# Performance work log

Hardware: AMD Instinct MI355X
Metric: run time of the kernel (lower is better)

Reference implementation:

```python
import jax, jax.numpy as jnp
import numpy as np

N_NODES = 50000
N_EDGES = 800000
IN_DIM = 128
HIDDEN = 64      # out_channels per head (concat=False -> head mean)
HEADS = 2
N_GRAPHS = 64
LN_EPS = 1e-5


def _layer_norm(x, g, b):
    mu = jnp.mean(x, axis=-1, keepdims=True)
    var = jnp.mean((x - mu) ** 2, axis=-1, keepdims=True)
    return (x - mu) * jax.lax.rsqrt(var + LN_EPS) * g + b


def _transformer_conv(x, src, dst, Wq, bq, Wk, bk, Wv, bv, Ws, bs):
    # PyG TransformerConv, concat=False, root_weight=True, beta=False.
    n = x.shape[0]
    q = (x @ Wq + bq).reshape(n, HEADS, -1)[dst]   # [E, H, D] query at target i
    k = (x @ Wk + bk).reshape(n, HEADS, -1)[src]   # [E, H, D] key at source j
    v = (x @ Wv + bv).reshape(n, HEADS, -1)[src]   # [E, H, D] value at source j
    d = q.shape[-1]
    score = jnp.sum(q * k, axis=-1) / jnp.sqrt(jnp.asarray(d, x.dtype))  # [E, H]
    # segment softmax over incoming edges of each target node
    smax = jax.ops.segment_max(score, dst, num_segments=n)
    e = jnp.exp(score - smax[dst])
    denom = jax.ops.segment_sum(e, dst, num_segments=n)
    alpha = e / denom[dst]                                              # [E, H]
    agg = jax.ops.segment_sum(alpha[..., None] * v, dst, num_segments=n)  # [N, H, D]
    out = jnp.mean(agg, axis=1)                     # concat=False -> head mean
    return out + x @ Ws + bs                        # root/skip connection


def setup_inputs() -> dict:
    key = jax.random.key(0)
    ks = jax.random.split(key, 40)
    inp = {}
    inp["x"] = jax.random.normal(ks[0], (N_NODES, IN_DIM), jnp.float32)
    inp["edge_index"] = jax.random.randint(ks[1], (2, N_EDGES), 0, N_NODES, dtype=jnp.int64)
    inp["batch"] = jnp.sort(jax.random.randint(ks[2], (N_NODES,), 0, N_GRAPHS, dtype=jnp.int64))
    dims = [(IN_DIM, HIDDEN), (HIDDEN, HIDDEN), (HIDDEN, HIDDEN)]
    i = 3
    for l, (din, dout) in enumerate(dims):
        for nm in ("q", "k", "v"):
            inp[f"W{nm}{l}"] = jax.random.normal(ks[i], (din, HEADS * dout), jnp.float32) * 0.05; i += 1
            inp[f"b{nm}{l}"] = jnp.zeros((HEADS * dout,), jnp.float32)
        inp[f"Ws{l}"] = jax.random.normal(ks[i], (din, dout), jnp.float32) * 0.05; i += 1
        inp[f"bs{l}"] = jnp.zeros((dout,), jnp.float32)
    for l in range(2):  # LayerNorm after layers 0 and 1 only
        inp[f"g{l}"] = jnp.ones((HIDDEN,), jnp.float32)
        inp[f"beta{l}"] = jnp.zeros((HIDDEN,), jnp.float32)
    inp["Wp"] = jax.random.normal(ks[i], (HIDDEN, 1), jnp.float32) * 0.05
    inp["bp"] = jnp.zeros((1,), jnp.float32)
    return inp


def reference(x, edge_index, batch,
              Wq0, bq0, Wk0, bk0, Wv0, bv0, Ws0, bs0,
              Wq1, bq1, Wk1, bk1, Wv1, bv1, Ws1, bs1,
              Wq2, bq2, Wk2, bk2, Wv2, bv2, Ws2, bs2,
              g0, beta0, g1, beta1, Wp, bp):
    src, dst = edge_index[0], edge_index[1]
    layers = [(Wq0, bq0, Wk0, bk0, Wv0, bv0, Ws0, bs0),
              (Wq1, bq1, Wk1, bk1, Wv1, bv1, Ws1, bs1),
              (Wq2, bq2, Wk2, bk2, Wv2, bv2, Ws2, bs2)]
    lns = [(g0, beta0), (g1, beta1)]
    h = x
    for i, p in enumerate(layers):
        h = _transformer_conv(h, src, dst, *p)
        h = jax.nn.relu(h)  # dropout p=0.0 / eval -> identity
        if i != len(layers) - 1:
            h = _layer_norm(h, *lns[i])
    # global mean pool per graph
    cnt = jax.ops.segment_sum(jnp.ones((h.shape[0],), h.dtype), batch, num_segments=N_GRAPHS)
    pooled = jax.ops.segment_sum(h, batch, num_segments=N_GRAPHS) / jnp.maximum(cnt, 1.0)[:, None]
    return pooled @ Wp + bp
```

## Files before the change

kernel.cpp:

```cpp
#include <hip/hip_runtime.h>
#include <hip/hip_fp16.h>
#include <math.h>

#define HIDDEN 64
#define HEADS 2
#define NCOLS 448
#define KV_COLS 256
#define N_GRAPHS 64
#define LN_EPS 1e-5f
#define Q_SCALE 0.18033688011112042f

typedef _Float16 half8 __attribute__((ext_vector_type(8)));
typedef _Float16 half2v __attribute__((ext_vector_type(2)));
typedef float    f32x4 __attribute__((ext_vector_type(4)));


__global__ void cast_f2h_kernel(const float* __restrict__ in, _Float16* __restrict__ out, int n4)
{
    int i = blockIdx.x * 256 + threadIdx.x;
    if (i < n4) {
        float4 v = *(const float4*)&in[i * 4];
        __half2 a = __floats2half2_rn(v.x, v.y);
        __half2 b = __floats2half2_rn(v.z, v.w);
        uint2 pk;
        pk.x = *(unsigned int*)&a;
        pk.y = *(unsigned int*)&b;
        *(uint2*)&out[i * 4] = pk;
    }
}

__global__ void pack_kernel(const float* __restrict__ Wq, const float* __restrict__ Wk,
                            const float* __restrict__ Wv, const float* __restrict__ Ws,
                            const float* __restrict__ bq, const float* __restrict__ bk,
                            const float* __restrict__ bv, const float* __restrict__ bs,
                            _Float16* __restrict__ Bt, float* __restrict__ bcat, int K)
{
    int idx = blockIdx.x * 256 + threadIdx.x;
    int total = NCOLS * K;
    if (idx < total) {
        int c = idx / K, k = idx - c * K;
        float v;
        if      (c < 128) v = Wq[k * 128 + c] * Q_SCALE;
        else if (c < 256) v = Wk[k * 128 + (c - 128)];
        else if (c < 384) v = Wv[k * 128 + (c - 256)];
        else              v = Ws[k * 64  + (c - 384)];
        Bt[idx] = (_Float16)v;
    }
    if (idx < NCOLS) {
        float b;
        if      (idx < 128) b = bq[idx] * Q_SCALE;
        else if (idx < 256) b = bk[idx - 128];
        else if (idx < 384) b = bv[idx - 256];
        else                b = bs[idx - 384];
        bcat[idx] = b;
    }
}

template<int K, int NT>
__device__ __forceinline__ void gemm_body(
    const _Float16* __restrict__ Ah, const float* __restrict__ bias,
    _Float16* __restrict__ qh, float* __restrict__ qsk, __half* __restrict__ kvh,
    const _Float16* Bs, int M, int colBase, int chunkRow0, int tid)
{
    int lane = tid & 63;
    int w    = tid >> 6;
    int fr   = lane & 15;
    int g    = lane >> 4;
    int row0 = chunkRow0 + w * 16;
    int arow = row0 + fr;
    if (arow > M - 1) arow = M - 1;

    f32x4 acc[NT];
    #pragma unroll
    for (int c = 0; c < NT; ++c) acc[c] = (f32x4){0.f, 0.f, 0.f, 0.f};

    #pragma unroll
    for (int ks = 0; ks < K / 32; ++ks) {
        int k0 = ks * 32 + g * 8;
        half8 af = *(const half8*)&Ah[(size_t)arow * K + k0];
        #pragma unroll
        for (int c = 0; c < NT; ++c) {
            int rl   = c * 16 + fr;
            int byte = rl * (K * 2) + k0 * 2;
            int sw   = byte ^ ((rl & 7) << 4);
            half8 bf = *(const half8*)((const char*)Bs + sw);
            acc[c] = __builtin_amdgcn_mfma_f32_16x16x32_f16(af, bf, acc[c], 0, 0, 0);
        }
    }

    #pragma unroll
    for (int c = 0; c < NT; ++c) {
        int col = colBase + c * 16 + fr;
        float bs = bias[col];
        #pragma unroll
        for (int j = 0; j < 4; ++j) {
            int row = row0 + g * 4 + j;
            if (row >= M) continue;
            float o = acc[c][j] + bs;
            if (col < 128) {
                qh[(size_t)row * 128 + col] = (_Float16)o;
            } else if (col >= 384) {
                qsk[(size_t)row * 64 + (col - 384)] = o;
            } else {
                int cc  = col - 128;
                int mat = cc >> 7;
                int hh  = (cc >> 6) & 1;
                int d   = cc & 63;
                int pos = mat * 128 + (d >> 2) * 8 + hh * 4 + (d & 3);
                kvh[(size_t)row * KV_COLS + pos] = __float2half_rn(o);
            }
        }
    }
}

template<int K>
__global__ __launch_bounds__(512, 4) void gemm_mfma_kernel(
    const _Float16* __restrict__ Ah,
    const _Float16* __restrict__ Bt,
    const float* __restrict__ bias,
    _Float16* __restrict__ qh, float* __restrict__ qsk,
    __half* __restrict__ kvh, int M)
{
    __shared__ _Float16 Bs[256 * K];

    int tid    = threadIdx.x;
    int colblk = blockIdx.x & 1;
    int chunk  = blockIdx.x >> 1;
    int colBase = colblk ? 256 : 0;
    int cols    = colblk ? 192 : 256;

    int bytes = cols * K * 2;
    const char* src = (const char*)Bt + (size_t)colBase * K * 2;
    for (int i = tid * 16; i < bytes; i += 512 * 16) {
        int rl = i / (K * 2);
        int sw = i ^ ((rl & 7) << 4);
        *(half8*)((char*)Bs + sw) = *(const half8*)(src + i);
    }
    __syncthreads();

    if (colblk == 0)
        gemm_body<K, 16>(Ah, bias, qh, qsk, kvh, Bs, M, 0,   chunk * 128, tid);
    else
        gemm_body<K, 12>(Ah, bias, qh, qsk, kvh, Bs, M, 256, chunk * 128, tid);
}

__global__ void hist_kernel(const int* __restrict__ dst, int* __restrict__ counts, int E)
{
    int i = blockIdx.x * 256 + threadIdx.x;
    if (i < E) atomicAdd(&counts[dst[i]], 1);
}

__global__ __launch_bounds__(256) void block_reduce_kernel(
    const int* __restrict__ counts, int* __restrict__ bsum, int N)
{
    __shared__ int s[256];
    int t = threadIdx.x;
    int i = blockIdx.x * 256 + t;
    s[t] = (i < N) ? counts[i] : 0;
    __syncthreads();
    #pragma unroll
    for (int o = 128; o; o >>= 1) {
        if (t < o) s[t] += s[t + o];
        __syncthreads();
    }
    if (t == 0) bsum[blockIdx.x] = s[0];
}

__global__ __launch_bounds__(256) void scan_partials_kernel(
    const int* __restrict__ bsum, int* __restrict__ boff, int nb, int* __restrict__ rowN)
{
    __shared__ int s[256];
    int t = threadIdx.x;
    int v = (t < nb) ? bsum[t] : 0;
    s[t] = v;
    __syncthreads();
    #pragma unroll
    for (int o = 1; o < 256; o <<= 1) {
        int x = (t >= o) ? s[t - o] : 0;
        __syncthreads();
        s[t] += x;
        __syncthreads();
    }
    if (t < nb) boff[t] = s[t] - v;
    if (t == nb - 1) rowN[0] = s[t];
}

__global__ __launch_bounds__(256) void block_scan_kernel(
    const int* __restrict__ counts, const int* __restrict__ boff,
    int* __restrict__ row_ptr, int* __restrict__ cursor, int N)
{
    __shared__ int s[256];
    int t = threadIdx.x;
    int i = blockIdx.x * 256 + t;
    int v = (i < N) ? counts[i] : 0;
    s[t] = v;
    __syncthreads();
    #pragma unroll
    for (int o = 1; o < 256; o <<= 1) {
        int x = (t >= o) ? s[t - o] : 0;
        __syncthreads();
        s[t] += x;
        __syncthreads();
    }
    if (i < N) {
        int excl = s[t] - v + boff[blockIdx.x];
        row_ptr[i] = excl;
        cursor[i]  = excl;
    }
}

__global__ void scatter_kernel(const int* __restrict__ ei, int* __restrict__ cursor,
                               int* __restrict__ src_sorted, int E)
{
    int i = blockIdx.x * 256 + threadIdx.x;
    if (i < E) {
        int d = ei[E + i];
        int pos = atomicAdd(&cursor[d], 1);
        src_sorted[pos] = ei[i];
    }
}

__device__ __forceinline__ float dpp_sum16(float x)
{
    float t;
    t = __int_as_float(__builtin_amdgcn_mov_dpp(__float_as_int(x), 0xB1,  0xF, 0xF, true)); x += t;
    t = __int_as_float(__builtin_amdgcn_mov_dpp(__float_as_int(x), 0x4E,  0xF, 0xF, true)); x += t;
    t = __int_as_float(__builtin_amdgcn_mov_dpp(__float_as_int(x), 0x141, 0xF, 0xF, true)); x += t;
    t = __int_as_float(__builtin_amdgcn_mov_dpp(__float_as_int(x), 0x140, 0xF, 0xF, true)); x += t;
    return x;
}

__global__ __launch_bounds__(256) void edge_conv_kernel(
    const _Float16* __restrict__ qh, const float* __restrict__ qsk,
    const __half* __restrict__ kvh,
    const int* __restrict__ row_ptr, const int* __restrict__ src_sorted,
    const float* __restrict__ gamma, const float* __restrict__ beta,
    float* __restrict__ hout, _Float16* __restrict__ hh, int N, int do_ln)
{
    int wave = threadIdx.x >> 6;
    int lane = threadIdx.x & 63;
    int g    = lane >> 4;
    int sub  = lane & 15;
    int node = blockIdx.x * 4 + wave;
    if (node >= N) return;

    const _Float16* qrow = qh + (size_t)node * 128;
    uint2 q0p = *(const uint2*)&qrow[sub * 4];
    uint2 q1p = *(const uint2*)&qrow[64 + sub * 4];
    const half2v* q0v = (const half2v*)&q0p;
    const half2v* q1v = (const half2v*)&q1p;

    int e0 = row_ptr[node], e1 = row_ptr[node + 1];
    int deg = e1 - e0;

    float  m0 = -1e30f, m1 = -1e30f;
    float  s0 = 0.f, s1 = 0.f;
    float4 a0 = make_float4(0.f, 0.f, 0.f, 0.f);
    float4 a1 = make_float4(0.f, 0.f, 0.f, 0.f);

    int  e    = e0 + g;
    bool have = (e < e1);
    uint4 kraw, vraw;
    if (have) {
        int j = src_sorted[e];
        const __half* jb = kvh + (size_t)j * KV_COLS;
        kraw = *(const uint4*)&jb[sub * 8];
        vraw = *(const uint4*)&jb[128 + sub * 8];
    }

    while (have) {
        int  en    = e + 4;
        bool haven = (en < e1);
        uint4 krn, vrn;
        if (haven) {
            int jn = src_sorted[en];
            const __half* jbn = kvh + (size_t)jn * KV_COLS;
            krn = *(const uint4*)&jbn[sub * 8];
            vrn = *(const uint4*)&jbn[128 + sub * 8];
        }

        const half2v* kh = (const half2v*)&kraw;
        float p0 = __builtin_amdgcn_fdot2(q0v[0], kh[0],
                     __builtin_amdgcn_fdot2(q0v[1], kh[1], 0.f, false), false);
        float p1 = __builtin_amdgcn_fdot2(q1v[0], kh[2],
                     __builtin_amdgcn_fdot2(q1v[1], kh[3], 0.f, false), false);
        float sc0 = dpp_sum16(p0);
        float sc1 = dpp_sum16(p1);

        const __half2* vp = (const __half2*)&vraw;
        float2 va = __half22float2(vp[0]), vb = __half22float2(vp[1]);
        float2 vc = __half22float2(vp[2]), vd = __half22float2(vp[3]);

        float nm0 = fmaxf(m0, sc0);
        float f0  = exp2f(m0 - nm0);
        float w0  = exp2f(sc0 - nm0);
        s0 = fmaf(s0, f0, w0);
        a0.x = fmaf(a0.x, f0, w0 * va.x);
        a0.y = fmaf(a0.y, f0, w0 * va.y);
        a0.z = fmaf(a0.z, f0, w0 * vb.x);
        a0.w = fmaf(a0.w, f0, w0 * vb.y);
        m0 = nm0;

        float nm1 = fmaxf(m1, sc1);
        float f1  = exp2f(m1 - nm1);
        float w1  = exp2f(sc1 - nm1);
        s1 = fmaf(s1, f1, w1);
        a1.x = fmaf(a1.x, f1, w1 * vc.x);
        a1.y = fmaf(a1.y, f1, w1 * vc.y);
        a1.z = fmaf(a1.z, f1, w1 * vd.x);
        a1.w = fmaf(a1.w, f1, w1 * vd.y);
        m1 = nm1;

        kraw = krn; vraw = vrn; e = en; have = haven;
    }

    #pragma unroll
    for (int offm = 16; offm <= 32; offm <<= 1) {
        float mo0 = __shfl_xor(m0, offm);
        float so0 = __shfl_xor(s0, offm);
        float4 ao0;
        ao0.x = __shfl_xor(a0.x, offm); ao0.y = __shfl_xor(a0.y, offm);
        ao0.z = __shfl_xor(a0.z, offm); ao0.w = __shfl_xor(a0.w, offm);
        float nm = fmaxf(m0, mo0);
        float fa = exp2f(m0 - nm), fb = exp2f(mo0 - nm);
        s0 = s0 * fa + so0 * fb;
        a0.x = a0.x * fa + ao0.x * fb; a0.y = a0.y * fa + ao0.y * fb;
        a0.z = a0.z * fa + ao0.z * fb; a0.w = a0.w * fa + ao0.w * fb;
        m0 = nm;

        float mo1 = __shfl_xor(m1, offm);
        float so1 = __shfl_xor(s1, offm);
        float4 ao1;
        ao1.x = __shfl_xor(a1.x, offm); ao1.y = __shfl_xor(a1.y, offm);
        ao1.z = __shfl_xor(a1.z, offm); ao1.w = __shfl_xor(a1.w, offm);
        nm = fmaxf(m1, mo1);
        fa = exp2f(m1 - nm); fb = exp2f(mo1 - nm);
        s1 = s1 * fa + so1 * fb;
        a1.x = a1.x * fa + ao1.x * fb; a1.y = a1.y * fa + ao1.y * fb;
        a1.z = a1.z * fa + ao1.z * fb; a1.w = a1.w * fa + ao1.w * fb;
        m1 = nm;
    }

    float4 skip = *(const float4*)&qsk[(size_t)node * 64 + sub * 4];
    float4 o;
    if (deg > 0) {
        float r0 = 0.5f / s0, r1 = 0.5f / s1;
        o.x = a0.x * r0 + a1.x * r1 + skip.x;
        o.y = a0.y * r0 + a1.y * r1 + skip.y;
        o.z = a0.z * r0 + a1.z * r1 + skip.z;
        o.w = a0.w * r0 + a1.w * r1 + skip.w;
    } else {
        o = skip;
    }
    o.x = fmaxf(o.x, 0.f); o.y = fmaxf(o.y, 0.f);
    o.z = fmaxf(o.z, 0.f); o.w = fmaxf(o.w, 0.f);

    if (do_ln) {
        float mu = dpp_sum16(o.x + o.y + o.z + o.w) * (1.0f / 64.0f);
        float dx = o.x - mu, dy = o.y - mu, dz = o.z - mu, dw = o.w - mu;
        float var = dpp_sum16(dx * dx + dy * dy + dz * dz + dw * dw) * (1.0f / 64.0f);
        float rs = rsqrtf(var + LN_EPS);
        float4 gm = *(const float4*)&gamma[sub * 4];
        float4 bt = *(const float4*)&beta[sub * 4];
        o.x = dx * rs * gm.x + bt.x;
        o.y = dy * rs * gm.y + bt.y;
        o.z = dz * rs * gm.z + bt.z;
        o.w = dw * rs * gm.w + bt.w;
    }
    if (g == 0) {
        *(float4*)&hout[(size_t)node * HIDDEN + sub * 4] = o;
        __half2 h01 = __floats2half2_rn(o.x, o.y);
        __half2 h23 = __floats2half2_rn(o.z, o.w);
        uint2 pk;
        pk.x = *(unsigned int*)&h01;
        pk.y = *(unsigned int*)&h23;
        *(uint2*)&hh[(size_t)node * HIDDEN + sub * 4] = pk;
    }
}

#define POOL_CHUNK 32
__global__ __launch_bounds__(64) void pool_kernel(const float* __restrict__ h,
                                                  const int* __restrict__ batch,
                                                  float* __restrict__ pooled,
                                                  float* __restrict__ cnt, int N)
{
    int lane = threadIdx.x;
    int start = blockIdx.x * POOL_CHUNK;
    if (start >= N) return;
    int end = min(start + POOL_CHUNK, N);
    int b0 = batch[start];
    int b1 = batch[end - 1];

    if (b0 == b1) {
        float acc = 0.f;
        #pragma unroll 4
        for (int i = start; i < end; ++i)
            acc += h[(size_t)i * HIDDEN + lane];
        atomicAdd(&pooled[b0 * HIDDEN + lane], acc);
        if (lane == 0) atomicAdd(&cnt[b0], (float)(end - start));
    } else {
        float acc = 0.f;
        int cur = b0, c = 0;
        for (int i = start; i < end; ++i) {
            int b = batch[i];
            if (b != cur) {
                atomicAdd(&pooled[cur * HIDDEN + lane], acc);
                if (lane == 0) atomicAdd(&cnt[cur], (float)c);
                acc = 0.f; c = 0; cur = b;
            }
            acc += h[(size_t)i * HIDDEN + lane];
            ++c;
        }
        atomicAdd(&pooled[cur * HIDDEN + lane], acc);
        if (lane == 0) atomicAdd(&cnt[cur], (float)c);
    }
}

__global__ void final_kernel(const float* __restrict__ pooled, const float* __restrict__ cnt,
                             const float* __restrict__ Wp, const float* __restrict__ bp,
                             float* __restrict__ out)
{
    int g = threadIdx.x;
    float c = fmaxf(cnt[g], 1.0f);
    float s = 0.f;
    for (int d = 0; d < HIDDEN; ++d) s += pooled[g * HIDDEN + d] * Wp[d];
    out[g] = s / c + bp[0];
}

extern "C" void kernel_launch(void* const* d_in, const int* in_sizes, int n_in,
                              void* d_out, int out_size, void* d_ws, size_t ws_size,
                              hipStream_t stream)
{
    const float* x    = (const float*)d_in[0];
    const int*   ei   = (const int*)d_in[1];
    const int*   batch= (const int*)d_in[2];

    const float* Wl[3][4];
    const float* bl[3][4];
    for (int l = 0; l < 3; ++l) {
        int b = 3 + l * 8;
        Wl[l][0] = (const float*)d_in[b + 0]; bl[l][0] = (const float*)d_in[b + 1];
        Wl[l][1] = (const float*)d_in[b + 2]; bl[l][1] = (const float*)d_in[b + 3];
        Wl[l][2] = (const float*)d_in[b + 4]; bl[l][2] = (const float*)d_in[b + 5];
        Wl[l][3] = (const float*)d_in[b + 6]; bl[l][3] = (const float*)d_in[b + 7];
    }
    const float* g0    = (const float*)d_in[27];
    const float* beta0 = (const float*)d_in[28];
    const float* g1    = (const float*)d_in[29];
    const float* beta1 = (const float*)d_in[30];
    const float* Wp    = (const float*)d_in[31];
    const float* bp    = (const float*)d_in[32];

    const int N = in_sizes[0] / 128;
    const int E = in_sizes[1] / 2;

    size_t off = 0;
    auto carve = [&](size_t bytes) -> char* {
        char* p = (char*)d_ws + off;
        off = (off + bytes + 255) & ~(size_t)255;
        return p;
    };
    _Float16*  qh     = (_Float16*)carve((size_t)N * 128 * 2);
    float*     qsk    = (float*)carve((size_t)N * 64 * 4);
    __half*    kvh    = (__half*)carve((size_t)N * KV_COLS * 2);
    float*     h      = (float*)carve((size_t)N * HIDDEN * 4);
    _Float16*  hh     = (_Float16*)carve((size_t)N * HIDDEN * 2);
    _Float16*  xh     = (_Float16*)carve((size_t)N * 128 * 2);
    _Float16*  Bt     = (_Float16*)carve((size_t)NCOLS * 128 * 2);
    float*     bcat   = (float*)carve(NCOLS * 4);
    int*       counts = (int*)carve((size_t)N * 4);
    int*       row_ptr= (int*)carve((size_t)(N + 1) * 4);
    int*       cursor = (int*)carve((size_t)N * 4);
    int*       src_sorted = (int*)carve((size_t)E * 4);
    int*       bsum   = (int*)carve(1024 * 4);
    int*       boff   = (int*)carve(1024 * 4);
    float*     pooled = (float*)carve((size_t)(N_GRAPHS * HIDDEN + N_GRAPHS) * 4);
    float*     cntf   = pooled + N_GRAPHS * HIDDEN;

    const int nb = (N + 255) / 256;

    hipMemsetAsync(counts, 0, (size_t)N * 4, stream);
    hist_kernel<<<(E + 255) / 256, 256, 0, stream>>>(ei + E, counts, E);
    block_reduce_kernel<<<nb, 256, 0, stream>>>(counts, bsum, N);
    scan_partials_kernel<<<1, 256, 0, stream>>>(bsum, boff, nb, &row_ptr[N]);
    block_scan_kernel<<<nb, 256, 0, stream>>>(counts, boff, row_ptr, cursor, N);
    scatter_kernel<<<(E + 255) / 256, 256, 0, stream>>>(ei, cursor, src_sorted, E);

    {
        int n4 = (N * 128) / 4;
        cast_f2h_kernel<<<(n4 + 255) / 256, 256, 0, stream>>>(x, xh, n4);
    }

    const int gemm_grid = 2 * ((N + 127) / 128);

    for (int l = 0; l < 3; ++l) {
        int K = (l == 0) ? 128 : 64;
        int packTot = NCOLS * K;
        pack_kernel<<<(packTot + 255) / 256, 256, 0, stream>>>(
            Wl[l][0], Wl[l][1], Wl[l][2], Wl[l][3],
            bl[l][0], bl[l][1], bl[l][2], bl[l][3], Bt, bcat, K);
        if (l == 0)
            gemm_mfma_kernel<128><<<gemm_grid, 512, 0, stream>>>(xh, Bt, bcat, qh, qsk, kvh, N);
        else
            gemm_mfma_kernel<64><<<gemm_grid, 512, 0, stream>>>(hh, Bt, bcat, qh, qsk, kvh, N);
        int do_ln = (l < 2) ? 1 : 0;
        const float* gg = (l == 0) ? g0 : g1;
        const float* bb = (l == 0) ? beta0 : beta1;
        edge_conv_kernel<<<(N + 3) / 4, 256, 0, stream>>>(
            qh, qsk, kvh, row_ptr, src_sorted, gg, bb, h, hh, N, do_ln);
    }

    hipMemsetAsync(pooled, 0, (size_t)(N_GRAPHS * HIDDEN + N_GRAPHS) * 4, stream);
    pool_kernel<<<(N + POOL_CHUNK - 1) / POOL_CHUNK, 64, 0, stream>>>(h, batch, pooled, cntf, N);
    final_kernel<<<1, 64, 0, stream>>>(pooled, cntf, Wp, bp, (float*)d_out);
}
```

Before: 421.3 us.

## Process nodes in descending-degree order and precompute byte offsets for KV gathers

Adds a degree counting-sort that builds a node order from high to low in-degree, and the edge kernel then processes nodes in that order so waves within a block do similar amounts of work and long nodes start first. Source indices are stored as precomputed byte offsets to save address arithmetic in the gather loop. The q·k dot product moves from packed fp16 fdot2 to fp32 FMAs after converting halves. This adds three small kernels plus a serial 64-entry offset pass, and gives up memory locality for q rows and the per-node outputs.

```diff
diff --git a/kernel.cpp b/kernel.cpp
--- a/kernel.cpp
+++ b/kernel.cpp
@@ -6,12 +6,12 @@
 #define HEADS 2
 #define NCOLS 448
 #define KV_COLS 256
+#define KV_ROW_BYTES 512
 #define N_GRAPHS 64
 #define LN_EPS 1e-5f
 #define Q_SCALE 0.18033688011112042f
 
 typedef _Float16 half8 __attribute__((ext_vector_type(8)));
-typedef _Float16 half2v __attribute__((ext_vector_type(2)));
 typedef float    f32x4 __attribute__((ext_vector_type(4)));
 
 
@@ -210,13 +210,52 @@
 }
 
 __global__ void scatter_kernel(const int* __restrict__ ei, int* __restrict__ cursor,
-                               int* __restrict__ src_sorted, int E)
+                               int* __restrict__ src_off, int E)
 {
     int i = blockIdx.x * 256 + threadIdx.x;
     if (i < E) {
         int d = ei[E + i];
         int pos = atomicAdd(&cursor[d], 1);
-        src_sorted[pos] = ei[i];
+        src_off[pos] = ei[i] * KV_ROW_BYTES;
+    }
+}
+
+__global__ __launch_bounds__(256) void deg_hist_kernel(
+    const int* __restrict__ row_ptr, int* __restrict__ dhist, int N)
+{
+    __shared__ int lh[64];
+    int t = threadIdx.x;
+    if (t < 64) lh[t] = 0;
+    __syncthreads();
+    int i = blockIdx.x * 256 + t;
+    if (i < N) {
+        int d = min(row_ptr[i + 1] - row_ptr[i], 63);
+        atomicAdd(&lh[d], 1);
+    }
+    __syncthreads();
+    if (t < 64 && lh[t] > 0) atomicAdd(&dhist[t], lh[t]);
+}
+
+__global__ void deg_offsets_kernel(const int* __restrict__ dhist, int* __restrict__ dcursor)
+{
+    if (threadIdx.x == 0) {
+        int off = 0;
+        for (int d = 63; d >= 0; --d) {
+            dcursor[d] = off;
+            off += dhist[d];
+        }
+    }
+}
+
+__global__ void deg_scatter_kernel(const int* __restrict__ row_ptr,
+                                   int* __restrict__ dcursor,
+                                   int* __restrict__ order, int N)
+{
+    int i = blockIdx.x * 256 + threadIdx.x;
+    if (i < N) {
+        int d = min(row_ptr[i + 1] - row_ptr[i], 63);
+        int pos = atomicAdd(&dcursor[d], 1);
+        order[pos] = i;
     }
 }
 
@@ -232,8 +271,8 @@
 
 __global__ __launch_bounds__(256) void edge_conv_kernel(
     const _Float16* __restrict__ qh, const float* __restrict__ qsk,
-    const __half* __restrict__ kvh,
-    const int* __restrict__ row_ptr, const int* __restrict__ src_sorted,
+    const __half* __restrict__ kvh, const int* __restrict__ order,
+    const int* __restrict__ row_ptr, const int* __restrict__ src_off,
     const float* __restrict__ gamma, const float* __restrict__ beta,
     float* __restrict__ hout, _Float16* __restrict__ hh, int N, int do_ln)
 {
@@ -241,14 +280,22 @@
     int lane = threadIdx.x & 63;
     int g    = lane >> 4;
     int sub  = lane & 15;
-    int node = blockIdx.x * 4 + wave;
-    if (node >= N) return;
-
-    const _Float16* qrow = qh + (size_t)node * 128;
-    uint2 q0p = *(const uint2*)&qrow[sub * 4];
-    uint2 q1p = *(const uint2*)&qrow[64 + sub * 4];
-    const half2v* q0v = (const half2v*)&q0p;
-    const half2v* q1v = (const half2v*)&q1p;
+    int idx  = blockIdx.x * 4 + wave;
+    if (idx >= N) return;
+    int node = order[idx];
+
+    const __half* qrow = (const __half*)(qh + (size_t)node * 128);
+    float4 q0, q1;
+    {
+        uint2 p0 = *(const uint2*)&qrow[sub * 4];
+        uint2 p1 = *(const uint2*)&qrow[64 + sub * 4];
+        const __half2* h0 = (const __half2*)&p0;
+        const __half2* h1 = (const __half2*)&p1;
+        float2 a = __half22float2(h0[0]), b = __half22float2(h0[1]);
+        float2 c = __half22float2(h1[0]), d = __half22float2(h1[1]);
+        q0 = make_float4(a.x, a.y, b.x, b.y);
+        q1 = make_float4(c.x, c.y, d.x, d.y);
+    }
 
     int e0 = row_ptr[node], e1 = row_ptr[node + 1];
     int deg = e1 - e0;
@@ -258,14 +305,14 @@
     float4 a0 = make_float4(0.f, 0.f, 0.f, 0.f);
     float4 a1 = make_float4(0.f, 0.f, 0.f, 0.f);
 
+    const char* kvb = (const char*)kvh;
     int  e    = e0 + g;
     bool have = (e < e1);
     uint4 kraw, vraw;
     if (have) {
-        int j = src_sorted[e];
-        const __half* jb = kvh + (size_t)j * KV_COLS;
-        kraw = *(const uint4*)&jb[sub * 8];
-        vraw = *(const uint4*)&jb[128 + sub * 8];
+        const char* jb = kvb + (size_t)(unsigned)src_off[e];
+        kraw = *(const uint4*)(jb + sub * 16);
+        vraw = *(const uint4*)(jb + 256 + sub * 16);
     }
 
     while (have) {
@@ -273,17 +320,17 @@
         bool haven = (en < e1);
         uint4 krn, vrn;
         if (haven) {
-            int jn = src_sorted[en];
-            const __half* jbn = kvh + (size_t)jn * KV_COLS;
-            krn = *(const uint4*)&jbn[sub * 8];
-            vrn = *(const uint4*)&jbn[128 + sub * 8];
+            const char* jbn = kvb + (size_t)(unsigned)src_off[en];
+            krn = *(const uint4*)(jbn + sub * 16);
+            vrn = *(const uint4*)(jbn + 256 + sub * 16);
         }
 
-        const half2v* kh = (const half2v*)&kraw;
-        float p0 = __builtin_amdgcn_fdot2(q0v[0], kh[0],
-                     __builtin_amdgcn_fdot2(q0v[1], kh[1], 0.f, false), false);
-        float p1 = __builtin_amdgcn_fdot2(q1v[0], kh[2],
-                     __builtin_amdgcn_fdot2(q1v[1], kh[3], 0.f, false), false);
+        const __half2* kp = (const __half2*)&kraw;
+        float2 ka = __half22float2(kp[0]), kb = __half22float2(kp[1]);
+        float2 kc = __half22float2(kp[2]), kd = __half22float2(kp[3]);
+
+        float p0 = fmaf(q0.w, kb.y, fmaf(q0.z, kb.x, fmaf(q0.y, ka.y, q0.x * ka.x)));
+        float p1 = fmaf(q1.w, kd.y, fmaf(q1.z, kd.x, fmaf(q1.y, kc.y, q1.x * kc.x)));
         float sc0 = dpp_sum16(p0);
         float sc1 = dpp_sum16(p1);
 
@@ -471,20 +518,28 @@
     int*       counts = (int*)carve((size_t)N * 4);
     int*       row_ptr= (int*)carve((size_t)(N + 1) * 4);
     int*       cursor = (int*)carve((size_t)N * 4);
-    int*       src_sorted = (int*)carve((size_t)E * 4);
+    int*       src_off = (int*)carve((size_t)E * 4);
+    int*       order  = (int*)carve((size_t)N * 4);
     int*       bsum   = (int*)carve(1024 * 4);
     int*       boff   = (int*)carve(1024 * 4);
+    int*       dhist  = (int*)carve(64 * 4);
+    int*       dcursor= (int*)carve(64 * 4);
     float*     pooled = (float*)carve((size_t)(N_GRAPHS * HIDDEN + N_GRAPHS) * 4);
     float*     cntf   = pooled + N_GRAPHS * HIDDEN;
 
     const int nb = (N + 255) / 256;
 
     hipMemsetAsync(counts, 0, (size_t)N * 4, stream);
+    hipMemsetAsync(dhist, 0, 64 * 4, stream);
     hist_kernel<<<(E + 255) / 256, 256, 0, stream>>>(ei + E, counts, E);
     block_reduce_kernel<<<nb, 256, 0, stream>>>(counts, bsum, N);
     scan_partials_kernel<<<1, 256, 0, stream>>>(bsum, boff, nb, &row_ptr[N]);
     block_scan_kernel<<<nb, 256, 0, stream>>>(counts, boff, row_ptr, cursor, N);
-    scatter_kernel<<<(E + 255) / 256, 256, 0, stream>>>(ei, cursor, src_sorted, E);
+    scatter_kernel<<<(E + 255) / 256, 256, 0, stream>>>(ei, cursor, src_off, E);
+
+    deg_hist_kernel<<<nb, 256, 0, stream>>>(row_ptr, dhist, N);
+    deg_offsets_kernel<<<1, 64, 0, stream>>>(dhist, dcursor);
+    deg_scatter_kernel<<<nb, 256, 0, stream>>>(row_ptr, dcursor, order, N);
 
     {
         int n4 = (N * 128) / 4;
@@ -507,7 +562,7 @@
         const float* gg = (l == 0) ? g0 : g1;
         const float* bb = (l == 0) ? beta0 : beta1;
         edge_conv_kernel<<<(N + 3) / 4, 256, 0, stream>>>(
-            qh, qsk, kvh, row_ptr, src_sorted, gg, bb, h, hh, N, do_ln);
+            qh, qsk, kvh, order, row_ptr, src_off, gg, bb, h, hh, N, do_ln);
     }
 
     hipMemsetAsync(pooled, 0, (size_t)(N_GRAPHS * HIDDEN + N_GRAPHS) * 4, stream);
```

Result: slower. 561.8 us (+33.4%).
